# Optimization experiments

Measured on AMD Instinct MI355X. Metric: run time of the kernel, lower is better.

The kernel has to match this reference:

```python
import jax, jax.numpy as jnp
import numpy as np

N, T, U, V = 8, 200, 50, 500
BLANK = 0
EPS = 1e-10


def setup_inputs() -> dict:
    key = jax.random.key(0)
    k1, k2, k3, k4, k5 = jax.random.split(key, 5)
    logits = jax.random.normal(k1, (N, T, U, V), jnp.float32)
    teacher_logits = jax.random.normal(k2, (N, T, U, V), jnp.float32)
    y = jax.random.randint(k3, (N, U), 1, V)            # padded labels (blank=0 used as pad)
    x_lens = jax.random.randint(k4, (N,), T // 2, T + 1)  # valid encoder frames
    y_lens = jax.random.randint(k5, (N,), U // 2, U + 1)  # valid label lengths
    return {"logits": logits, "teacher_logits": teacher_logits, "y": y,
            "x_lens": x_lens, "y_lens": y_lens}


def reference(logits, teacher_logits, y, x_lens, y_lens):
    # Efficient RNNT-KD: collapse V-dim softmax into 3 classes (label, blank, rest).
    n, t, u, v = logits.shape
    s = jax.nn.softmax(logits, axis=-1)             # (N,T,U,V)
    te = jax.nn.softmax(teacher_logits, axis=-1)    # (N,T,U,V)

    idx = jnp.broadcast_to(y[:, None, :, None], (n, t, u, 1))  # label index per (n,t,u)
    py = jnp.take_along_axis(s, idx, axis=-1)       # (N,T,U,1)
    t_py = jnp.take_along_axis(te, idx, axis=-1)
    blank = s[..., BLANK:BLANK + 1]
    t_blank = te[..., BLANK:BLANK + 1]

    rem = 1.0 - py - blank
    t_rem = 1.0 - t_py - t_blank
    t_rem = jnp.where(t_rem < 0, EPS, t_rem)        # floor negative remainders (in-place set in torch)

    student = jnp.log(jnp.clip(jnp.concatenate([py, blank, rem], axis=-1), EPS, 1.0))  # (N,T,U,3)
    teacher = jnp.concatenate([t_py, t_blank, t_rem], axis=-1)                          # (N,T,U,3)

    t_mask = (jnp.arange(t)[None, :] < x_lens[:, None]).astype(student.dtype)[:, :, None, None]
    u_mask = (jnp.arange(u)[None, :] < y_lens[:, None]).astype(student.dtype)[:, None, :, None]
    m = t_mask * u_mask
    return jnp.stack([student * m, teacher * m])    # (2,N,T,U,3)
```

## Files before the change

kernel.cpp:

```cpp
#include <hip/hip_runtime.h>

#define N_ 8
#define T_ 200
#define U_ 50
#define V_ 500
#define NTU (N_ * T_ * U_)
#define EPSF 1e-10f

__global__ __launch_bounds__(256) void tkd_kernel(
    const float* __restrict__ lg,
    const float* __restrict__ tl,
    const int* __restrict__ y,
    const int* __restrict__ xlen,
    const int* __restrict__ ylen,
    float* __restrict__ out)
{
    const int wid  = (int)((blockIdx.x * 256 + threadIdx.x) >> 6);
    const int lane = threadIdx.x & 63;
    if (wid >= NTU) return;

    const int n  = wid / (T_ * U_);
    const int r2 = wid - n * (T_ * U_);
    const int t  = r2 / U_;
    const int u  = r2 - t * U_;

    const size_t base  = (size_t)wid * V_;
    const int    start = lane * 8;

    const float NI = -INFINITY;
    float4 a0 = make_float4(NI, NI, NI, NI), a1 = a0, b0 = a0, b1 = a0;
    if (start + 4 <= V_) {
        a0 = *reinterpret_cast<const float4*>(lg + base + start);
        b0 = *reinterpret_cast<const float4*>(tl + base + start);
    }
    if (start + 8 <= V_) {
        a1 = *reinterpret_cast<const float4*>(lg + base + start + 4);
        b1 = *reinterpret_cast<const float4*>(tl + base + start + 4);
    }

    float a[8] = {a0.x, a0.y, a0.z, a0.w, a1.x, a1.y, a1.z, a1.w};
    float b[8] = {b0.x, b0.y, b0.z, b0.w, b1.x, b1.y, b1.z, b1.w};

    float sA = 0.f, sB = 0.f;
#pragma unroll
    for (int j = 0; j < 8; ++j) {
        sA += __expf(a[j]);
        sB += __expf(b[j]);
    }
#pragma unroll
    for (int off = 32; off > 0; off >>= 1) {
        sA += __shfl_xor(sA, off, 64);
        sB += __shfl_xor(sB, off, 64);
    }

    const int yv = y[n * U_ + u];
    const int reg = yv & 7;
    float selA = a[0], selB = b[0];
#pragma unroll
    for (int j = 1; j < 8; ++j) {
        if (reg == j) { selA = a[j]; selB = b[j]; }
    }
    const float ay  = __shfl(selA, yv >> 3, 64);
    const float by  = __shfl(selB, yv >> 3, 64);
    const float av0 = __shfl(a[0], 0, 64);
    const float bv0 = __shfl(b[0], 0, 64);

    const float invA = 1.0f / sA;
    const float invB = 1.0f / sB;
    const float py    = __expf(ay)  * invA;
    const float pbl   = __expf(av0) * invA;
    const float prem  = 1.0f - py - pbl;
    const float tpy   = __expf(by)  * invB;
    const float tbl   = __expf(bv0) * invB;
    float trem  = 1.0f - tpy - tbl;
    if (trem < 0.0f) trem = EPSF;

    const float s0 = __logf(fminf(fmaxf(py,   EPSF), 1.0f));
    const float s1 = __logf(fminf(fmaxf(pbl,  EPSF), 1.0f));
    const float s2 = __logf(fminf(fmaxf(prem, EPSF), 1.0f));

    const float mm = ((t < xlen[n]) && (u < ylen[n])) ? 1.0f : 0.0f;

    if (lane == 0) {
        const size_t o = (size_t)wid * 3;
        out[o + 0] = s0 * mm;
        out[o + 1] = s1 * mm;
        out[o + 2] = s2 * mm;
        const size_t o2 = (size_t)NTU * 3 + o;
        out[o2 + 0] = tpy  * mm;
        out[o2 + 1] = tbl  * mm;
        out[o2 + 2] = trem * mm;
    }
}

extern "C" void kernel_launch(void* const* d_in, const int* in_sizes, int n_in,
                              void* d_out, int out_size, void* d_ws, size_t ws_size,
                              hipStream_t stream) {
    const float* lg = (const float*)d_in[0];
    const float* tl = (const float*)d_in[1];
    const int* y    = (const int*)d_in[2];
    const int* xlen = (const int*)d_in[3];
    const int* ylen = (const int*)d_in[4];
    float* out = (float*)d_out;

    const int blocks = (NTU + 3) / 4;
    tkd_kernel<<<blocks, 256, 0, stream>>>(lg, tl, y, xlen, ylen, out);
}
```

Before: 319.9 us.

## Process each row with 16 lanes instead of a full wavefront

```diff
diff --git a/kernel.cpp b/kernel.cpp
--- a/kernel.cpp
+++ b/kernel.cpp
@@ -15,74 +15,72 @@
     const int* __restrict__ ylen,
     float* __restrict__ out)
 {
-    const int wid  = (int)((blockIdx.x * 256 + threadIdx.x) >> 6);
-    const int lane = threadIdx.x & 63;
-    if (wid >= NTU) return;
+    const int tid = threadIdx.x;
+    const int l   = tid & 15;
+    const int row = blockIdx.x * 16 + (tid >> 4);
 
-    const int n  = wid / (T_ * U_);
-    const int r2 = wid - n * (T_ * U_);
+    const int n  = row / (T_ * U_);
+    const int r2 = row - n * (T_ * U_);
     const int t  = r2 / U_;
     const int u  = r2 - t * U_;
 
-    const size_t base  = (size_t)wid * V_;
-    const int    start = lane * 8;
+    const size_t base = (size_t)row * V_;
+    const float4* pa = reinterpret_cast<const float4*>(lg + base);
+    const float4* pb = reinterpret_cast<const float4*>(tl + base);
 
+    float4 A[8], B[8];
+#pragma unroll
+    for (int j = 0; j < 7; ++j) {
+        A[j] = pa[j * 16 + l];
+        B[j] = pb[j * 16 + l];
+    }
     const float NI = -INFINITY;
-    float4 a0 = make_float4(NI, NI, NI, NI), a1 = a0, b0 = a0, b1 = a0;
-    if (start + 4 <= V_) {
-        a0 = *reinterpret_cast<const float4*>(lg + base + start);
-        b0 = *reinterpret_cast<const float4*>(tl + base + start);
-    }
-    if (start + 8 <= V_) {
-        a1 = *reinterpret_cast<const float4*>(lg + base + start + 4);
-        b1 = *reinterpret_cast<const float4*>(tl + base + start + 4);
+    A[7] = make_float4(NI, NI, NI, NI);
+    B[7] = A[7];
+    if (l <= 12) {
+        A[7] = pa[112 + l];
+        B[7] = pb[112 + l];
     }
 
-    float a[8] = {a0.x, a0.y, a0.z, a0.w, a1.x, a1.y, a1.z, a1.w};
-    float b[8] = {b0.x, b0.y, b0.z, b0.w, b1.x, b1.y, b1.z, b1.w};
+    const int   yv = y[n * U_ + u];
+    const float ay = lg[base + yv];
+    const float by = tl[base + yv];
+    const float a0 = lg[base];
+    const float b0 = tl[base];
 
     float sA = 0.f, sB = 0.f;
 #pragma unroll
     for (int j = 0; j < 8; ++j) {
-        sA += __expf(a[j]);
-        sB += __expf(b[j]);
+        sA += __expf(A[j].x); sA += __expf(A[j].y);
+        sA += __expf(A[j].z); sA += __expf(A[j].w);
+        sB += __expf(B[j].x); sB += __expf(B[j].y);
+        sB += __expf(B[j].z); sB += __expf(B[j].w);
     }
+
 #pragma unroll
-    for (int off = 32; off > 0; off >>= 1) {
+    for (int off = 1; off < 16; off <<= 1) {
         sA += __shfl_xor(sA, off, 64);
         sB += __shfl_xor(sB, off, 64);
     }
 
-    const int yv = y[n * U_ + u];
-    const int reg = yv & 7;
-    float selA = a[0], selB = b[0];
-#pragma unroll
-    for (int j = 1; j < 8; ++j) {
-        if (reg == j) { selA = a[j]; selB = b[j]; }
-    }
-    const float ay  = __shfl(selA, yv >> 3, 64);
-    const float by  = __shfl(selB, yv >> 3, 64);
-    const float av0 = __shfl(a[0], 0, 64);
-    const float bv0 = __shfl(b[0], 0, 64);
+    if (l == 0) {
+        const float invA = 1.0f / sA;
+        const float invB = 1.0f / sB;
+        const float py   = __expf(ay) * invA;
+        const float pbl  = __expf(a0) * invA;
+        const float prem = 1.0f - py - pbl;
+        const float tpy  = __expf(by) * invB;
+        const float tbl  = __expf(b0) * invB;
+        float trem = 1.0f - tpy - tbl;
+        if (trem < 0.0f) trem = EPSF;
 
-    const float invA = 1.0f / sA;
-    const float invB = 1.0f / sB;
-    const float py    = __expf(ay)  * invA;
-    const float pbl   = __expf(av0) * invA;
-    const float prem  = 1.0f - py - pbl;
-    const float tpy   = __expf(by)  * invB;
-    const float tbl   = __expf(bv0) * invB;
-    float trem  = 1.0f - tpy - tbl;
-    if (trem < 0.0f) trem = EPSF;
+        const float s0 = __logf(fminf(fmaxf(py,   EPSF), 1.0f));
+        const float s1 = __logf(fminf(fmaxf(pbl,  EPSF), 1.0f));
+        const float s2 = __logf(fminf(fmaxf(prem, EPSF), 1.0f));
 
-    const float s0 = __logf(fminf(fmaxf(py,   EPSF), 1.0f));
-    const float s1 = __logf(fminf(fmaxf(pbl,  EPSF), 1.0f));
-    const float s2 = __logf(fminf(fmaxf(prem, EPSF), 1.0f));
+        const float mm = ((t < xlen[n]) && (u < ylen[n])) ? 1.0f : 0.0f;
 
-    const float mm = ((t < xlen[n]) && (u < ylen[n])) ? 1.0f : 0.0f;
-
-    if (lane == 0) {
-        const size_t o = (size_t)wid * 3;
+        const size_t o = (size_t)row * 3;
         out[o + 0] = s0 * mm;
         out[o + 1] = s1 * mm;
         out[o + 2] = s2 * mm;
@@ -103,6 +101,5 @@
     const int* ylen = (const int*)d_in[4];
     float* out = (float*)d_out;
 
-    const int blocks = (NTU + 3) / 4;
-    tkd_kernel<<<blocks, 256, 0, stream>>>(lg, tl, y, xlen, ylen, out);
+    tkd_kernel<<<NTU / 16, 256, 0, stream>>>(lg, tl, y, xlen, ylen, out);
 }
```

Measured after the change: 325.3 us. About the same (+1.7%).
